# Optimization experiments

Hardware: AMD Instinct MI355X
Metric: run time of the kernel (lower is better)

Reference implementation:

```python
import jax, jax.numpy as jnp
import numpy as np

N_NODES = 100000
N_EDGES = 1600000
D_IN, D_H, D_OUT = 128, 128, 40
BN_EPS = 1e-5


def _glorot(k, shape):
    lim = float(np.sqrt(6.0 / (shape[0] + shape[1])))
    return jax.random.uniform(k, shape, jnp.float32, -lim, lim)


def setup_inputs() -> dict:
    key = jax.random.key(0)
    ks = jax.random.split(key, 8)
    return {
        "x": jax.random.normal(ks[0], (N_NODES, D_IN), jnp.float32),
        "edge_index": jax.random.randint(ks[1], (2, N_EDGES), 0, N_NODES, jnp.int32),
        "w1": _glorot(ks[2], (D_IN, D_H)), "r1": _glorot(ks[3], (D_IN, D_H)),
        "b1": jnp.zeros((D_H,), jnp.float32),
        "g1": jnp.ones((D_H,), jnp.float32), "be1": jnp.zeros((D_H,), jnp.float32),
        "w2": _glorot(ks[4], (D_H, D_H)), "r2": _glorot(ks[5], (D_H, D_H)),
        "b2": jnp.zeros((D_H,), jnp.float32),
        "g2": jnp.ones((D_H,), jnp.float32), "be2": jnp.zeros((D_H,), jnp.float32),
        "w3": _glorot(ks[6], (D_H, D_OUT)), "r3": _glorot(ks[7], (D_H, D_OUT)),
        "b3": jnp.zeros((D_OUT,), jnp.float32),
    }


def _sage_conv(x, src, dst, w, r, b, n_nodes):
    # mean aggregation over incoming edges: adj.matmul(x, reduce='mean')
    agg = jax.ops.segment_sum(x[src], dst, num_segments=n_nodes)  # [N, D]
    deg = jax.ops.segment_sum(jnp.ones_like(src, dtype=x.dtype), dst, num_segments=n_nodes)
    mean = agg / jnp.maximum(deg, 1.0)[:, None]
    return mean @ w + x @ r + b


def _batch_norm(h, gamma, beta):
    # training-mode BN over node dim (batch statistics)
    mu = h.mean(axis=0)
    var = h.var(axis=0)
    return (h - mu) * jax.lax.rsqrt(var + BN_EPS) * gamma + beta


def reference(x, edge_index, w1, r1, b1, g1, be1, w2, r2, b2, g2, be2, w3, r3, b3):
    n = x.shape[0]
    src, dst = edge_index[0], edge_index[1]
    h = _sage_conv(x, src, dst, w1, r1, b1, n)
    h = jax.nn.relu(_batch_norm(h, g1, be1))
    h = _sage_conv(h, src, dst, w2, r2, b2, n)
    h = jax.nn.relu(_batch_norm(h, g2, be2))
    h = _sage_conv(h, src, dst, w3, r3, b3, n)
    return jax.nn.log_softmax(h, axis=-1)
```

## Files before the change

kernel.cpp:

```cpp
#include <hip/hip_runtime.h>
#include <cstdint>
#include <cstddef>
#include <math.h>

#define N_NODES 100000
#define N_EDGES 1600000
#define DIM 128
#define DOUT 40
#define BN_EPS 1e-5f

#define NB 500
#define NPB 200
#define BCAP 4096
#define BKT_BLOCKS 800
#define EPB (N_EDGES / BKT_BLOCKS)

typedef __attribute__((ext_vector_type(8))) short bf16x8;
typedef __attribute__((ext_vector_type(4))) float f32x4;

__device__ __forceinline__ float bf2f(uint u16shifted) {
    union { uint i; float f; } c; c.i = u16shifted; return c.f;
}
__device__ __forceinline__ ushort f2bf(float f) {
    union { float f; uint i; } c; c.f = f;
    uint i = c.i;
    uint lsb = (i >> 16) & 1u;
    i += 0x7FFFu + lsb;
    return (ushort)(i >> 16);
}
__device__ __forceinline__ uint bnpack(uint u, float s0, float h0, float s1, float h1) {
    float lo = fmaxf(bf2f(u << 16) * s0 + h0, 0.f);
    float hi = fmaxf(bf2f(u & 0xFFFF0000u) * s1 + h1, 0.f);
    return (uint)f2bf(lo) | ((uint)f2bf(hi) << 16);
}

__device__ __forceinline__ void wcat_body(const float* __restrict__ W,
                                          const float* __restrict__ R,
                                          ushort* __restrict__ out, int NW, int blk) {
    int idx = blk * 256 + threadIdx.x;
    int n = idx >> 8, k = idx & 255;
    float v = 0.f;
    if (n < NW) v = (k < 128) ? W[k * NW + n] : R[(k - 128) * NW + n];
    int fc = n >> 4, l15 = n & 15;
    int ks = k >> 5, lhi = (k & 31) >> 3, j = k & 7;
    out[(fc * 8 + ks) * 512 + (lhi * 16 + l15) * 8 + j] = f2bf(v);
}

__global__ __launch_bounds__(256) void k_prep(const float* __restrict__ x,
                                              ushort* __restrict__ Xb,
                                              const float* __restrict__ w1, const float* __restrict__ r1, ushort* __restrict__ Wc1,
                                              const float* __restrict__ w2, const float* __restrict__ r2, ushort* __restrict__ Wc2,
                                              const float* __restrict__ w3, const float* __restrict__ r3, ushort* __restrict__ Wc3,
                                              const int* __restrict__ ei,
                                              uint* __restrict__ bucketbuf,
                                              int* __restrict__ gcnt) {
    int b = blockIdx.x;
    int tid = threadIdx.x;
    if (b < BKT_BLOCKS) {
        __shared__ int hist[NB];
        __shared__ int base_[NB];
        for (int i = tid; i < NB; i += 256) hist[i] = 0;
        __syncthreads();
        int e0 = b * EPB, e1 = e0 + EPB;
        for (int e = e0 + tid; e < e1; e += 256) {
            int d = ei[N_EDGES + e];
            atomicAdd(&hist[d / NPB], 1);
        }
        __syncthreads();
        for (int i = tid; i < NB; i += 256) base_[i] = atomicAdd(&gcnt[i], hist[i]);
        __syncthreads();
        for (int i = tid; i < NB; i += 256) hist[i] = 0;
        __syncthreads();
        for (int e = e0 + tid; e < e1; e += 256) {
            int d = ei[N_EDGES + e];
            int s = ei[e];
            int bk = d / NPB;
            int pos = base_[bk] + atomicAdd(&hist[bk], 1);
            if (pos < BCAP)
                bucketbuf[(size_t)bk * BCAP + pos] = ((uint)(d - bk * NPB) << 17) | (uint)s;
        }
    } else if (b < BKT_BLOCKS + 128) {
        wcat_body(w1, r1, Wc1, 128, b - BKT_BLOCKS);
    } else if (b < BKT_BLOCKS + 256) {
        wcat_body(w2, r2, Wc2, 128, b - (BKT_BLOCKS + 128));
    } else if (b < BKT_BLOCKS + 304) {
        wcat_body(w3, r3, Wc3, DOUT, b - (BKT_BLOCKS + 256));
    } else {
        int n4 = N_NODES * DIM / 4;
        int i = (b - (BKT_BLOCKS + 304)) * 256 + tid;
        int stride = 2048 * 256;
        for (; i < n4; i += stride) {
            float4 v = reinterpret_cast<const float4*>(x)[i];
            ushort4 o;
            o.x = f2bf(v.x); o.y = f2bf(v.y); o.z = f2bf(v.z); o.w = f2bf(v.w);
            reinterpret_cast<ushort4*>(Xb)[i] = o;
        }
    }
}

__global__ __launch_bounds__(256) void k_csr_build(const int* __restrict__ ei,
                                                   const uint* __restrict__ bucketbuf,
                                                   const int* __restrict__ gcnt,
                                                   int* __restrict__ rowstart,
                                                   int* __restrict__ csr) {
    __shared__ int cnts[NPB + 1];
    __shared__ int lcur[NPB];
    __shared__ int csr_l[BCAP];
    __shared__ int baseS;
    int b = blockIdx.x, tid = threadIdx.x;
    int cnt = gcnt[b];
    int lo = b * NPB;
    if (tid == 0) baseS = 0;
    for (int i = tid; i < NPB; i += 256) cnts[i] = 0;
    __syncthreads();
    int part = 0;
    for (int i = tid; i < b; i += 256) part += gcnt[i];
    if (part) atomicAdd(&baseS, part);
    bool fits = (cnt <= BCAP);
    if (fits) {
        for (int i = tid; i < cnt; i += 256)
            atomicAdd(&cnts[bucketbuf[(size_t)b * BCAP + i] >> 17], 1);
    } else {
        for (int e = tid; e < N_EDGES; e += 256) {
            int d = ei[N_EDGES + e];
            if (d >= lo && d < lo + NPB) atomicAdd(&cnts[d - lo], 1);
        }
    }
    __syncthreads();
    int base = baseS;
    if (tid == 0) {
        int run = 0;
        for (int i = 0; i < NPB; i++) { int c = cnts[i]; cnts[i] = run; run += c; }
        cnts[NPB] = run;
    }
    __syncthreads();
    for (int i = tid; i < NPB; i += 256) rowstart[lo + i] = base + cnts[i];
    if (b == NB - 1 && tid == 0) rowstart[N_NODES] = N_EDGES;
    for (int i = tid; i < NPB; i += 256) lcur[i] = 0;
    __syncthreads();
    if (fits) {
        for (int i = tid; i < cnt; i += 256) {
            uint p = bucketbuf[(size_t)b * BCAP + i];
            int dl = p >> 17;
            int pos = cnts[dl] + atomicAdd(&lcur[dl], 1);
            csr_l[pos] = (int)(p & 0x1FFFFu);
        }
        __syncthreads();
        for (int i = tid; i < cnt; i += 256) csr[base + i] = csr_l[i];
    } else {
        for (int e = tid; e < N_EDGES; e += 256) {
            int d = ei[N_EDGES + e];
            if (d >= lo && d < lo + NPB) {
                int dl = d - lo;
                int pos = cnts[dl] + atomicAdd(&lcur[dl], 1);
                csr[base + pos] = ei[e];
            }
        }
    }
}

__global__ __launch_bounds__(256) void k_bnrelu(ushort* __restrict__ H,
                                                const float* __restrict__ stats,
                                                const float* __restrict__ g,
                                                const float* __restrict__ be) {
    __shared__ float scS[128], shS[128];
    int tid = threadIdx.x;
    if (tid < 128) {
        float mu = stats[tid] * (1.0f / N_NODES);
        float var = stats[128 + tid] * (1.0f / N_NODES) - mu * mu;
        float sc = g[tid] * rsqrtf(var + BN_EPS);
        scS[tid] = sc;
        shS[tid] = be[tid] - mu * sc;
    }
    __syncthreads();
    uint4* H4 = reinterpret_cast<uint4*>(H);
    const int total = N_NODES * 16;
    for (int i = blockIdx.x * 256 + tid; i < total; i += gridDim.x * 256) {
        uint4 u = H4[i];
        int c0 = (i & 15) * 8;
        u.x = bnpack(u.x, scS[c0 + 0], shS[c0 + 0], scS[c0 + 1], shS[c0 + 1]);
        u.y = bnpack(u.y, scS[c0 + 2], shS[c0 + 2], scS[c0 + 3], shS[c0 + 3]);
        u.z = bnpack(u.z, scS[c0 + 4], shS[c0 + 4], scS[c0 + 5], shS[c0 + 5]);
        u.w = bnpack(u.w, scS[c0 + 6], shS[c0 + 6], scS[c0 + 7], shS[c0 + 7]);
        H4[i] = u;
    }
}

__global__ __launch_bounds__(256) void k_agg_bf(const ushort* __restrict__ cur,
                                                const int* __restrict__ rowstart,
                                                const int* __restrict__ csr,
                                                ushort* __restrict__ out) {
    int wid = (blockIdx.x * blockDim.x + threadIdx.x) >> 6;
    int lane = threadIdx.x & 63;
    if (wid >= N_NODES) return;
    int beg = rowstart[wid];
    int end = rowstart[wid + 1];
    int slot = lane >> 4;
    int cg = lane & 15;
    const uint4* base = reinterpret_cast<const uint4*>(cur);
    float a0 = 0.f, a1 = 0.f, a2 = 0.f, a3 = 0.f, a4 = 0.f, a5 = 0.f, a6 = 0.f, a7 = 0.f;
#pragma unroll 2
    for (int e = beg + slot; e < end; e += 4) {
        int s = csr[e];
        uint4 u = base[(size_t)s * 16 + cg];
        a0 += bf2f(u.x << 16); a1 += bf2f(u.x & 0xFFFF0000u);
        a2 += bf2f(u.y << 16); a3 += bf2f(u.y & 0xFFFF0000u);
        a4 += bf2f(u.z << 16); a5 += bf2f(u.z & 0xFFFF0000u);
        a6 += bf2f(u.w << 16); a7 += bf2f(u.w & 0xFFFF0000u);
    }
#pragma unroll
    for (int off = 16; off < 64; off <<= 1) {
        a0 += __shfl_xor(a0, off, 64); a1 += __shfl_xor(a1, off, 64);
        a2 += __shfl_xor(a2, off, 64); a3 += __shfl_xor(a3, off, 64);
        a4 += __shfl_xor(a4, off, 64); a5 += __shfl_xor(a5, off, 64);
        a6 += __shfl_xor(a6, off, 64); a7 += __shfl_xor(a7, off, 64);
    }
    if (slot == 0) {
        int deg = end - beg;
        float inv = 1.0f / (float)(deg > 1 ? deg : 1);
        uint4 o;
        o.x = (uint)f2bf(a0 * inv) | ((uint)f2bf(a1 * inv) << 16);
        o.y = (uint)f2bf(a2 * inv) | ((uint)f2bf(a3 * inv) << 16);
        o.z = (uint)f2bf(a4 * inv) | ((uint)f2bf(a5 * inv) << 16);
        o.w = (uint)f2bf(a6 * inv) | ((uint)f2bf(a7 * inv) << 16);
        reinterpret_cast<uint4*>(out)[(size_t)wid * 16 + cg] = o;
    }
}

__global__ __launch_bounds__(256, 2) void k_gemm_mfma(const ushort* __restrict__ Am,
                                                      const ushort* __restrict__ Ac,
                                                      const ushort* __restrict__ Wcat,
                                                      const float* __restrict__ bias,
                                                      ushort* __restrict__ out,
                                                      float* __restrict__ stats_out,
                                                      int dostats) {
    __shared__ ushort A2[2][128][136];
    __shared__ float lsum[128], lsumsq[128];
    int tid = threadIdx.x;
    int wid = tid >> 6, lane = tid & 63;
    int wr = wid >> 1, wc = wid & 1;
    int l15 = lane & 15, lhi = lane >> 4;
    int row0 = blockIdx.x * 128;

    if (tid < 128) { lsum[tid] = 0.f; lsumsq[tid] = 0.f; }

    for (int h = 0; h < 2; ++h) {
        const ushort* Asrc = h ? Ac : Am;
#pragma unroll
        for (int i = 0; i < 8; ++i) {
            int idx = i * 256 + tid;
            int row = idx >> 4, q = idx & 15;
            int gr = row0 + row;
            uint4 v = {0, 0, 0, 0};
            if (gr < N_NODES)
                v = *reinterpret_cast<const uint4*>(Asrc + (size_t)gr * 128 + q * 8);
            *reinterpret_cast<uint4*>(&A2[h][row][q * 8]) = v;
        }
    }
    __syncthreads();

    f32x4 acc[4][4];
#pragma unroll
    for (int m = 0; m < 4; m++)
#pragma unroll
        for (int n = 0; n < 4; n++) acc[m][n] = (f32x4){0.f, 0.f, 0.f, 0.f};

#pragma unroll
    for (int ks = 0; ks < 8; ++ks) {
        int kg = ks * 32;
        int half = kg >> 7;
        int ka = (kg & 127) + lhi * 8;
        bf16x8 a[4], b[4];
#pragma unroll
        for (int m = 0; m < 4; m++)
            a[m] = *reinterpret_cast<bf16x8*>(&A2[half][wr * 64 + m * 16 + l15][ka]);
#pragma unroll
        for (int n = 0; n < 4; n++)
            b[n] = *reinterpret_cast<const bf16x8*>(Wcat + ((wc * 4 + n) * 8 + ks) * 512 + lane * 8);
#pragma unroll
        for (int m = 0; m < 4; m++)
#pragma unroll
            for (int n = 0; n < 4; n++)
                acc[m][n] = __builtin_amdgcn_mfma_f32_16x16x32_bf16(a[m], b[n], acc[m][n], 0, 0, 0);
    }
    float ps[4] = {0.f, 0.f, 0.f, 0.f}, ps2[4] = {0.f, 0.f, 0.f, 0.f};
#pragma unroll
    for (int m = 0; m < 4; m++) {
        int rbase = row0 + wr * 64 + m * 16 + lhi * 4;
#pragma unroll
        for (int n = 0; n < 4; n++) {
            int col = wc * 64 + n * 16 + l15;
            float bv = bias[col];
#pragma unroll
            for (int j = 0; j < 4; j++) {
                int gr = rbase + j;
                if (gr < N_NODES) {
                    float v = acc[m][n][j] + bv;
                    out[(size_t)gr * 128 + col] = f2bf(v);
                    ps[n] += v;
                    ps2[n] += v * v;
                }
            }
        }
    }
    if (dostats) {
#pragma unroll
        for (int n = 0; n < 4; n++) {
            ps[n] += __shfl_xor(ps[n], 16, 64);
            ps2[n] += __shfl_xor(ps2[n], 16, 64);
            ps[n] += __shfl_xor(ps[n], 32, 64);
            ps2[n] += __shfl_xor(ps2[n], 32, 64);
        }
        if (lhi == 0) {
#pragma unroll
            for (int n = 0; n < 4; n++) {
                int col = wc * 64 + n * 16 + l15;
                atomicAdd(&lsum[col], ps[n]);
                atomicAdd(&lsumsq[col], ps2[n]);
            }
        }
        __syncthreads();
        if (tid < 128) {
            atomicAdd(&stats_out[tid], lsum[tid]);
            atomicAdd(&stats_out[128 + tid], lsumsq[tid]);
        }
    }
}

__global__ __launch_bounds__(256, 2) void k_gemm40_mfma(const ushort* __restrict__ Am,
                                                        const ushort* __restrict__ Ac,
                                                        const ushort* __restrict__ Wcat,
                                                        const float* __restrict__ bias,
                                                        float* __restrict__ out) {
    __shared__ ushort A2[2][128][136];
    int tid = threadIdx.x;
    int w = tid >> 6, lane = tid & 63;
    int l15 = lane & 15, lhi = lane >> 4;
    int row0 = blockIdx.x * 128;

    for (int h = 0; h < 2; ++h) {
        const ushort* Asrc = h ? Ac : Am;
#pragma unroll
        for (int i = 0; i < 8; ++i) {
            int idx = i * 256 + tid;
            int row = idx >> 4, q = idx & 15;
            int gr = row0 + row;
            uint4 v = {0, 0, 0, 0};
            if (gr < N_NODES)
                v = *reinterpret_cast<const uint4*>(Asrc + (size_t)gr * 128 + q * 8);
            *reinterpret_cast<uint4*>(&A2[h][row][q * 8]) = v;
        }
    }
    __syncthreads();

    f32x4 acc[2][3];
#pragma unroll
    for (int m = 0; m < 2; m++)
#pragma unroll
        for (int n = 0; n < 3; n++) acc[m][n] = (f32x4){0.f, 0.f, 0.f, 0.f};

#pragma unroll
    for (int ks = 0; ks < 8; ++ks) {
        int kg = ks * 32;
        int half = kg >> 7;
        int ka = (kg & 127) + lhi * 8;
        bf16x8 a[2], b[3];
#pragma unroll
        for (int m = 0; m < 2; m++)
            a[m] = *reinterpret_cast<bf16x8*>(&A2[half][w * 32 + m * 16 + l15][ka]);
#pragma unroll
        for (int n = 0; n < 3; n++)
            b[n] = *reinterpret_cast<const bf16x8*>(Wcat + (n * 8 + ks) * 512 + lane * 8);
#pragma unroll
        for (int m = 0; m < 2; m++)
#pragma unroll
            for (int n = 0; n < 3; n++)
                acc[m][n] = __builtin_amdgcn_mfma_f32_16x16x32_bf16(a[m], b[n], acc[m][n], 0, 0, 0);
    }
    float b0 = bias[l15];
    float b1 = bias[16 + l15];
    float b2 = (l15 < 8) ? bias[32 + l15] : 0.f;
#pragma unroll
    for (int m = 0; m < 2; m++) {
#pragma unroll
        for (int j = 0; j < 4; j++) {
            int grow = row0 + w * 32 + m * 16 + lhi * 4 + j;
            float v0 = acc[m][0][j] + b0;
            float v1 = acc[m][1][j] + b1;
            float v2 = (l15 < 8) ? (acc[m][2][j] + b2) : -INFINITY;
            float mx = fmaxf(fmaxf(v0, v1), v2);
#pragma unroll
            for (int off = 1; off < 16; off <<= 1) mx = fmaxf(mx, __shfl_xor(mx, off, 64));
            float s = expf(v0 - mx) + expf(v1 - mx) + ((l15 < 8) ? expf(v2 - mx) : 0.f);
#pragma unroll
            for (int off = 1; off < 16; off <<= 1) s += __shfl_xor(s, off, 64);
            float lg = mx + logf(s);
            if (grow < N_NODES) {
                out[(size_t)grow * DOUT + l15] = v0 - lg;
                out[(size_t)grow * DOUT + 16 + l15] = v1 - lg;
                if (l15 < 8) out[(size_t)grow * DOUT + 32 + l15] = v2 - lg;
            }
        }
    }
}

extern "C" void kernel_launch(void* const* d_in, const int* in_sizes, int n_in,
                              void* d_out, int out_size, void* d_ws, size_t ws_size,
                              hipStream_t stream) {
    const float* x = (const float*)d_in[0];
    const int* ei = (const int*)d_in[1];
    const float* w1 = (const float*)d_in[2];
    const float* r1 = (const float*)d_in[3];
    const float* b1 = (const float*)d_in[4];
    const float* g1 = (const float*)d_in[5];
    const float* be1 = (const float*)d_in[6];
    const float* w2 = (const float*)d_in[7];
    const float* r2 = (const float*)d_in[8];
    const float* b2 = (const float*)d_in[9];
    const float* g2 = (const float*)d_in[10];
    const float* be2 = (const float*)d_in[11];
    const float* w3 = (const float*)d_in[12];
    const float* r3 = (const float*)d_in[13];
    const float* b3 = (const float*)d_in[14];
    float* out = (float*)d_out;

    const size_t NF = (size_t)N_NODES * DIM;
    ushort* Xb = (ushort*)d_ws;
    ushort* Ab = Xb + NF;
    ushort* Bb = Ab + NF;
    ushort* Wc1 = Bb + NF;
    ushort* Wc2 = Wc1 + 128 * 256;
    ushort* Wc3 = Wc2 + 128 * 256;
    uint* bucketbuf = (uint*)(Wc3 + 48 * 256);
    int* gcnt = (int*)(bucketbuf + (size_t)NB * BCAP);
    float* statsA = (float*)(gcnt + NB);
    float* statsB = statsA + 256;
    int* rowstart = (int*)(statsB + 256);
    int* csr = rowstart + (N_NODES + 1);
    size_t needed = (size_t)((char*)(csr + N_EDGES) - (char*)d_ws);
    if (ws_size < needed) return;

    const int AGG_BLOCKS = N_NODES / 4;
    const int GEMM_BLOCKS = (N_NODES + 127) / 128;
    const int PREP_BLOCKS = BKT_BLOCKS + 304 + 2048;

    hipMemsetAsync(gcnt, 0, (NB + 512) * sizeof(int), stream);
    k_prep<<<PREP_BLOCKS, 256, 0, stream>>>(x, Xb, w1, r1, Wc1, w2, r2, Wc2, w3, r3, Wc3,
                                            ei, bucketbuf, gcnt);
    k_csr_build<<<NB, 256, 0, stream>>>(ei, bucketbuf, gcnt, rowstart, csr);

    k_agg_bf<<<AGG_BLOCKS, 256, 0, stream>>>(Xb, rowstart, csr, Ab);
    k_gemm_mfma<<<GEMM_BLOCKS, 256, 0, stream>>>(Ab, Xb, Wc1, b1, Ab, statsA, 1);
    k_bnrelu<<<2048, 256, 0, stream>>>(Ab, statsA, g1, be1);

    k_agg_bf<<<AGG_BLOCKS, 256, 0, stream>>>(Ab, rowstart, csr, Bb);
    k_gemm_mfma<<<GEMM_BLOCKS, 256, 0, stream>>>(Bb, Ab, Wc2, b2, Bb, statsB, 1);
    k_bnrelu<<<2048, 256, 0, stream>>>(Bb, statsB, g2, be2);

    k_agg_bf<<<AGG_BLOCKS, 256, 0, stream>>>(Bb, rowstart, csr, Ab);
    k_gemm40_mfma<<<GEMM_BLOCKS, 256, 0, stream>>>(Ab, Bb, Wc3, b3, out);
}
```

Baseline: 376.7 us.

## Overlap second A-half load with MFMA in GEMMs; shrink bucketing blocks

In both MFMA GEMM kernels, the concatenated operand's second half is now loaded into registers while the first-half MFMA loop runs. It is then written to shared memory behind an extra barrier, so global latency overlaps compute. The prep kernel uses fewer bucketing blocks, each handling more edges, and reorders block roles so the bf16 conversion blocks come before the weight-concat blocks. The register staging raises VGPR pressure (8 uint4 per thread), which may affect occupancy under launch_bounds(256,2). Fewer bucketing blocks reduce global atomic contention on gcnt but cut parallelism.

```diff
diff --git a/kernel.cpp b/kernel.cpp
--- a/kernel.cpp
+++ b/kernel.cpp
@@ -12,7 +12,7 @@
 #define NB 500
 #define NPB 200
 #define BCAP 4096
-#define BKT_BLOCKS 800
+#define BKT_BLOCKS 200
 #define EPB (N_EDGES / BKT_BLOCKS)
 
 typedef __attribute__((ext_vector_type(8))) short bf16x8;
@@ -79,15 +79,9 @@
             if (pos < BCAP)
                 bucketbuf[(size_t)bk * BCAP + pos] = ((uint)(d - bk * NPB) << 17) | (uint)s;
         }
-    } else if (b < BKT_BLOCKS + 128) {
-        wcat_body(w1, r1, Wc1, 128, b - BKT_BLOCKS);
-    } else if (b < BKT_BLOCKS + 256) {
-        wcat_body(w2, r2, Wc2, 128, b - (BKT_BLOCKS + 128));
-    } else if (b < BKT_BLOCKS + 304) {
-        wcat_body(w3, r3, Wc3, DOUT, b - (BKT_BLOCKS + 256));
-    } else {
+    } else if (b < BKT_BLOCKS + 2048) {
         int n4 = N_NODES * DIM / 4;
-        int i = (b - (BKT_BLOCKS + 304)) * 256 + tid;
+        int i = (b - BKT_BLOCKS) * 256 + tid;
         int stride = 2048 * 256;
         for (; i < n4; i += stride) {
             float4 v = reinterpret_cast<const float4*>(x)[i];
@@ -95,6 +89,12 @@
             o.x = f2bf(v.x); o.y = f2bf(v.y); o.z = f2bf(v.z); o.w = f2bf(v.w);
             reinterpret_cast<ushort4*>(Xb)[i] = o;
         }
+    } else if (b < BKT_BLOCKS + 2048 + 128) {
+        wcat_body(w1, r1, Wc1, 128, b - (BKT_BLOCKS + 2048));
+    } else if (b < BKT_BLOCKS + 2048 + 256) {
+        wcat_body(w2, r2, Wc2, 128, b - (BKT_BLOCKS + 2048 + 128));
+    } else {
+        wcat_body(w3, r3, Wc3, DOUT, b - (BKT_BLOCKS + 2048 + 256));
     }
 }
 
@@ -244,18 +244,26 @@
 
     if (tid < 128) { lsum[tid] = 0.f; lsumsq[tid] = 0.f; }
 
-    for (int h = 0; h < 2; ++h) {
-        const ushort* Asrc = h ? Ac : Am;
-#pragma unroll
-        for (int i = 0; i < 8; ++i) {
-            int idx = i * 256 + tid;
-            int row = idx >> 4, q = idx & 15;
-            int gr = row0 + row;
-            uint4 v = {0, 0, 0, 0};
-            if (gr < N_NODES)
-                v = *reinterpret_cast<const uint4*>(Asrc + (size_t)gr * 128 + q * 8);
-            *reinterpret_cast<uint4*>(&A2[h][row][q * 8]) = v;
-        }
+#pragma unroll
+    for (int i = 0; i < 8; ++i) {
+        int idx = i * 256 + tid;
+        int row = idx >> 4, q = idx & 15;
+        int gr = row0 + row;
+        uint4 v = {0, 0, 0, 0};
+        if (gr < N_NODES)
+            v = *reinterpret_cast<const uint4*>(Am + (size_t)gr * 128 + q * 8);
+        *reinterpret_cast<uint4*>(&A2[0][row][q * 8]) = v;
+    }
+    uint4 sreg[8];
+#pragma unroll
+    for (int i = 0; i < 8; ++i) {
+        int idx = i * 256 + tid;
+        int row = idx >> 4, q = idx & 15;
+        int gr = row0 + row;
+        uint4 v = {0, 0, 0, 0};
+        if (gr < N_NODES)
+            v = *reinterpret_cast<const uint4*>(Ac + (size_t)gr * 128 + q * 8);
+        sreg[i] = v;
     }
     __syncthreads();
 
@@ -266,14 +274,35 @@
         for (int n = 0; n < 4; n++) acc[m][n] = (f32x4){0.f, 0.f, 0.f, 0.f};
 
 #pragma unroll
-    for (int ks = 0; ks < 8; ++ks) {
-        int kg = ks * 32;
-        int half = kg >> 7;
-        int ka = (kg & 127) + lhi * 8;
+    for (int ks = 0; ks < 4; ++ks) {
+        int ka = ks * 32 + lhi * 8;
         bf16x8 a[4], b[4];
 #pragma unroll
         for (int m = 0; m < 4; m++)
-            a[m] = *reinterpret_cast<bf16x8*>(&A2[half][wr * 64 + m * 16 + l15][ka]);
+            a[m] = *reinterpret_cast<bf16x8*>(&A2[0][wr * 64 + m * 16 + l15][ka]);
+#pragma unroll
+        for (int n = 0; n < 4; n++)
+            b[n] = *reinterpret_cast<const bf16x8*>(Wcat + ((wc * 4 + n) * 8 + ks) * 512 + lane * 8);
+#pragma unroll
+        for (int m = 0; m < 4; m++)
+#pragma unroll
+            for (int n = 0; n < 4; n++)
+                acc[m][n] = __builtin_amdgcn_mfma_f32_16x16x32_bf16(a[m], b[n], acc[m][n], 0, 0, 0);
+    }
+#pragma unroll
+    for (int i = 0; i < 8; ++i) {
+        int idx = i * 256 + tid;
+        int row = idx >> 4, q = idx & 15;
+        *reinterpret_cast<uint4*>(&A2[1][row][q * 8]) = sreg[i];
+    }
+    __syncthreads();
+#pragma unroll
+    for (int ks = 4; ks < 8; ++ks) {
+        int ka = (ks - 4) * 32 + lhi * 8;
+        bf16x8 a[4], b[4];
+#pragma unroll
+        for (int m = 0; m < 4; m++)
+            a[m] = *reinterpret_cast<bf16x8*>(&A2[1][wr * 64 + m * 16 + l15][ka]);
 #pragma unroll
         for (int n = 0; n < 4; n++)
             b[n] = *reinterpret_cast<const bf16x8*>(Wcat + ((wc * 4 + n) * 8 + ks) * 512 + lane * 8);
@@ -338,18 +367,26 @@
     int l15 = lane & 15, lhi = lane >> 4;
     int row0 = blockIdx.x * 128;
 
-    for (int h = 0; h < 2; ++h) {
-        const ushort* Asrc = h ? Ac : Am;
-#pragma unroll
-        for (int i = 0; i < 8; ++i) {
-            int idx = i * 256 + tid;
-            int row = idx >> 4, q = idx & 15;
-            int gr = row0 + row;
-            uint4 v = {0, 0, 0, 0};
-            if (gr < N_NODES)
-                v = *reinterpret_cast<const uint4*>(Asrc + (size_t)gr * 128 + q * 8);
-            *reinterpret_cast<uint4*>(&A2[h][row][q * 8]) = v;
-        }
+#pragma unroll
+    for (int i = 0; i < 8; ++i) {
+        int idx = i * 256 + tid;
+        int row = idx >> 4, q = idx & 15;
+        int gr = row0 + row;
+        uint4 v = {0, 0, 0, 0};
+        if (gr < N_NODES)
+            v = *reinterpret_cast<const uint4*>(Am + (size_t)gr * 128 + q * 8);
+        *reinterpret_cast<uint4*>(&A2[0][row][q * 8]) = v;
+    }
+    uint4 sreg[8];
+#pragma unroll
+    for (int i = 0; i < 8; ++i) {
+        int idx = i * 256 + tid;
+        int row = idx >> 4, q = idx & 15;
+        int gr = row0 + row;
+        uint4 v = {0, 0, 0, 0};
+        if (gr < N_NODES)
+            v = *reinterpret_cast<const uint4*>(Ac + (size_t)gr * 128 + q * 8);
+        sreg[i] = v;
     }
     __syncthreads();
 
@@ -360,14 +397,35 @@
         for (int n = 0; n < 3; n++) acc[m][n] = (f32x4){0.f, 0.f, 0.f, 0.f};
 
 #pragma unroll
-    for (int ks = 0; ks < 8; ++ks) {
-        int kg = ks * 32;
-        int half = kg >> 7;
-        int ka = (kg & 127) + lhi * 8;
+    for (int ks = 0; ks < 4; ++ks) {
+        int ka = ks * 32 + lhi * 8;
         bf16x8 a[2], b[3];
 #pragma unroll
         for (int m = 0; m < 2; m++)
-            a[m] = *reinterpret_cast<bf16x8*>(&A2[half][w * 32 + m * 16 + l15][ka]);
+            a[m] = *reinterpret_cast<bf16x8*>(&A2[0][w * 32 + m * 16 + l15][ka]);
+#pragma unroll
+        for (int n = 0; n < 3; n++)
+            b[n] = *reinterpret_cast<const bf16x8*>(Wcat + (n * 8 + ks) * 512 + lane * 8);
+#pragma unroll
+        for (int m = 0; m < 2; m++)
+#pragma unroll
+            for (int n = 0; n < 3; n++)
+                acc[m][n] = __builtin_amdgcn_mfma_f32_16x16x32_bf16(a[m], b[n], acc[m][n], 0, 0, 0);
+    }
+#pragma unroll
+    for (int i = 0; i < 8; ++i) {
+        int idx = i * 256 + tid;
+        int row = idx >> 4, q = idx & 15;
+        *reinterpret_cast<uint4*>(&A2[1][row][q * 8]) = sreg[i];
+    }
+    __syncthreads();
+#pragma unroll
+    for (int ks = 4; ks < 8; ++ks) {
+        int ka = (ks - 4) * 32 + lhi * 8;
+        bf16x8 a[2], b[3];
+#pragma unroll
+        for (int m = 0; m < 2; m++)
+            a[m] = *reinterpret_cast<bf16x8*>(&A2[1][w * 32 + m * 16 + l15][ka]);
 #pragma unroll
         for (int n = 0; n < 3; n++)
             b[n] = *reinterpret_cast<const bf16x8*>(Wcat + (n * 8 + ks) * 512 + lane * 8);
@@ -442,7 +500,7 @@
 
     const int AGG_BLOCKS = N_NODES / 4;
     const int GEMM_BLOCKS = (N_NODES + 127) / 128;
-    const int PREP_BLOCKS = BKT_BLOCKS + 304 + 2048;
+    const int PREP_BLOCKS = BKT_BLOCKS + 2048 + 304;
 
     hipMemsetAsync(gcnt, 0, (NB + 512) * sizeof(int), stream);
     k_prep<<<PREP_BLOCKS, 256, 0, stream>>>(x, Xb, w1, r1, Wc1, w2, r2, Wc2, w3, r3, Wc3,
```

New measurement: 369.6 us. About the same (-1.9%).
